# Optimization experiments

Measured on AMD Instinct MI355X. Metric: run time of the kernel, lower is better.

## Reference

```python
import math
import jax, jax.numpy as jnp
import numpy as np


def _scharr(img):
    # img: (..., H, W) -> (..., 2, H, W); F.conv2d is cross-correlation, as is lax.conv
    kx = jnp.array([[-3., 0., 3.], [10., 0., 10.], [-3., 0., 3.]], jnp.float32)
    k = jnp.stack([kx, kx.T])[:, None]  # (2,1,3,3)
    lead = img.shape[:-2]
    x = img.reshape((-1, 1) + img.shape[-2:])
    y = jax.lax.conv_general_dilated(x, k, (1, 1), 'SAME',
                                     dimension_numbers=('NCHW', 'OIHW', 'NCHW'))
    return y.reshape(lead + (2,) + img.shape[-2:])


def _rotate_nearest(x, angle_deg):
    # torchvision-style rotate with expand=True, nearest interpolation, zero fill
    H, W = x.shape[-2], x.shape[-1]
    a = math.radians(angle_deg)
    c, s = math.cos(a), math.sin(a)
    Hn = int(math.ceil(abs(W * s) + abs(H * c)))
    Wn = int(math.ceil(abs(W * c) + abs(H * s)))
    yy, xx = jnp.meshgrid(jnp.arange(Hn, dtype=jnp.float32),
                          jnp.arange(Wn, dtype=jnp.float32), indexing='ij')
    xg = xx - (Wn - 1) / 2.0
    yg = yy - (Hn - 1) / 2.0
    xi = c * xg - s * yg + (W - 1) / 2.0
    yi = s * xg + c * yg + (H - 1) / 2.0
    xn = jnp.round(xi).astype(jnp.int32)
    yn = jnp.round(yi).astype(jnp.int32)
    valid = (xn >= 0) & (xn < W) & (yn >= 0) & (yn < H)
    out = x[..., jnp.clip(yn, 0, H - 1), jnp.clip(xn, 0, W - 1)]
    return jnp.where(valid, out, jnp.zeros((), x.dtype))


def _gauss_derivs(img):
    # image_gaussian_derivatives: (B, C, H, W) -> (B, C, 8, H, W)
    H, W = img.shape[-2:]
    g = _scharr(img)  # (B, C, 2, H, W)
    # rotated_xywh(H, W, 45) to get crop offsets, exactly as in the source
    a = math.radians(45.0)
    al, be = math.cos(a), math.sin(a)
    cx, cy = W / 2.0, H / 2.0
    pts = [(0., 0.), (W - 1., 0.), (0., H - 1.), (W - 1., H - 1.)]
    rx = [al * px + be * py + (1 - al) * cx - be * cy for px, py in pts]
    ry = [-be * px + al * py + be * cx + (1 - al) * cy for px, py in pts]
    w45 = max(rx) - min(rx)
    h45 = max(ry) - min(ry)
    startx = int(max(0, (w45 - W) / 2))
    starty = int(max(0, (h45 - H) / 2))
    gr = _scharr(_rotate_nearest(img, 45.0))      # (B, C, 2, Hr, Wr)
    grb = _rotate_nearest(gr, -45.0)
    grc = grb[..., starty:starty + H, startx:startx + W]  # (B, C, 2, H, W)
    return jnp.concatenate([jnp.clip(g, 0, None), jnp.clip(g, None, 0),
                            jnp.clip(grc, 0, None), jnp.clip(grc, None, 0)], axis=-3)


def _normalize_min_max(x):
    hmin = x.min(axis=(-2, -1), keepdims=True)
    hmax = x.max(axis=(-2, -1), keepdims=True)
    return (x - hmin) / (hmax - hmin)


def _batched_hist(Z, nbins):
    # Z: (..., N) int in [0, nbins) -> per-row histogram (..., nbins) via one fused segment_sum
    lead = Z.shape[:-1]
    L = int(np.prod(lead))
    Zf = Z.reshape(L, -1)
    ids = (jnp.arange(L, dtype=jnp.int32)[:, None] * nbins + Zf).ravel()
    h = jax.ops.segment_sum(jnp.ones(ids.shape, jnp.float32), ids, num_segments=L * nbins)
    return h.reshape(lead + (nbins,))


def setup_inputs() -> dict:
    key = jax.random.key(0)
    k1, k2 = jax.random.split(key)
    img = jax.random.uniform(k1, (2, 3, 512, 512), jnp.float32)
    reg_lab = jax.random.randint(k2, (2, 1, 3, 512, 512), 0, 256, dtype=jnp.int32)
    return {'img': img, 'reg_lab': reg_lab,
            'color_bins': 25, 'texture_bins': 10, 'num_segments': 256}


def reference(img, reg_lab, color_bins, texture_bins, num_segments):
    B, I, G, H, W = reg_lab.shape
    C = img.shape[1]
    S = num_segments
    # normalized oriented gradient features (B, C, 8, H, W)
    tex = _normalize_min_max(_gauss_derivs(img))
    # region sizes: scatter_add of ones over region labels
    region_sizes = _batched_hist(reg_lab.reshape(B, I, G, H * W), S)  # (B,I,G,S)
    # color histograms
    Zc = (reg_lab[:, :, :, None].astype(jnp.float32) * color_bins
          + img[:, None, None] * (color_bins - 1)).astype(jnp.int32)  # (B,I,G,C,H,W)
    ch = _batched_hist(Zc.reshape(B, I, G, C, H * W), S * color_bins)
    ch = jnp.moveaxis(ch.reshape(B, I, G, C, S, color_bins), -2, -3)  # (B,I,G,S,C,cb)
    ch = ch / ch.sum(axis=(-2, -1), keepdims=True)
    # texture histograms
    Zt = (reg_lab[:, :, :, None, None].astype(jnp.float32) * texture_bins
          + tex[:, None, None] * (texture_bins - 1)).astype(jnp.int32)  # (B,I,G,C,8,H,W)
    th = _batched_hist(Zt.reshape(B, I, G, C, 8, H * W), S * texture_bins)
    th = jnp.moveaxis(th.reshape(B, I, G, C, 8, S, texture_bins), -2, -4)  # (B,I,G,S,C,8,tb)
    th = th / th.sum(axis=(-3, -2, -1), keepdims=True)
    # per-region bounding boxes via segment min/max (replaces the 5-deep python loop)
    grid_y, grid_x = jnp.meshgrid(jnp.arange(H, dtype=jnp.int32),
                                  jnp.arange(W, dtype=jnp.int32), indexing='ij')
    BIG = B * I * G
    ids = (jnp.arange(BIG, dtype=jnp.int32)[:, None] * S
           + reg_lab.reshape(BIG, H * W)).ravel()
    xs = jnp.tile(grid_x.ravel(), BIG)
    ys = jnp.tile(grid_y.ravel(), BIG)
    n = BIG * S
    xmin = jax.ops.segment_min(xs, ids, num_segments=n)
    xmax = jax.ops.segment_max(xs, ids, num_segments=n)
    ymin = jax.ops.segment_min(ys, ids, num_segments=n)
    ymax = jax.ops.segment_max(ys, ids, num_segments=n)
    nonempty = region_sizes.reshape(n) > 0
    xmin = jnp.where(nonempty, xmin, W)
    ymin = jnp.where(nonempty, ymin, H)
    xmax = jnp.where(nonempty, xmax, 0)
    ymax = jnp.where(nonempty, ymax, 0)
    xywh = jnp.stack([xmin, ymin, xmax - xmin, ymax - ymin], axis=-1).reshape(B, I, G, S, 4)
    return region_sizes, ch, th, xywh
```

## Files before the change

kernel.cpp:

```cpp
#include <hip/hip_runtime.h>
#include <climits>

#define HW 262144
#define IW 512
#define RN 725
#define NSEG 256
#define CH_OFF 1536
#define TH_OFF 116736
#define XY_OFF 485376
#define NBLK 256
#define THP 24
#define CHP 32

#define ASTR 67
#define RSTR 73
#define ROFF 156

static __device__ __forceinline__ float rtap_l(const float* __restrict__ Rt,
                                               int rx0, int ry0, int cx, int cy) {
    if (cx < 0 || cx >= RN || cy < 0 || cy >= RN) return 0.f;
    const float cs = 0.7071067811865476f;
    float xg = (float)cx - 362.0f;
    float yg = (float)cy - 362.0f;
    float xi = cs * xg - cs * yg + 255.5f;
    float yi = cs * xg + cs * yg + 255.5f;
    int xs = (int)rintf(xi);
    int ys = (int)rintf(yi);
    if (xs < 0 || xs >= IW || ys < 0 || ys >= IW) return 0.f;
    return Rt[(ys - ry0) * RSTR + (xs - rx0)];
}

static __device__ __forceinline__ void mm_of_map(const float* __restrict__ pmin,
                                                 const float* __restrict__ pmax,
                                                 int m, float* slo, float* shi,
                                                 float& mn, float& mx) {
    int tid = threadIdx.x;
    float lo = 3.4e38f, hi = -3.4e38f;
    for (int i = tid; i < NBLK; i += 256) {
        lo = fminf(lo, pmin[m * NBLK + i]);
        hi = fmaxf(hi, pmax[m * NBLK + i]);
    }
    slo[tid] = lo; shi[tid] = hi;
    __syncthreads();
    for (int off = 128; off > 0; off >>= 1) {
        if (tid < off) {
            slo[tid] = fminf(slo[tid], slo[tid + off]);
            shi[tid] = fmaxf(shi[tid], shi[tid + off]);
        }
        __syncthreads();
    }
    mn = slo[0]; mx = shi[0];
    __syncthreads();
}

__global__ __launch_bounds__(256) void k_front(
    const float* __restrict__ img, const int* __restrict__ lab,
    float* __restrict__ gmaps, float* __restrict__ pmin, float* __restrict__ pmax,
    unsigned char* __restrict__ lab8, unsigned* __restrict__ chp_w,
    unsigned* __restrict__ rsp, int* __restrict__ bxmin, int* __restrict__ bxmax,
    int* __restrict__ bymin, int* __restrict__ bymax)
{
    __shared__ __align__(16) unsigned char smem[20480];
    int bxid = blockIdx.x;
    int tid = threadIdx.x;
    int grp = bxid / 11, rem = bxid % 11;
    if (rem < 8) {
        int u = grp * 8 + rem;
        int tile = u & 255;
        int bc = u >> 8;
        float* At = (float*)smem;
        float* Rt = At + 18 * ASTR;
        float (*slo)[256] = (float (*)[256])(Rt + 24 * RSTR);
        float (*shi)[256] = slo + 4;
        {
            int i = tile * 256 + tid;
            int4 l = ((const int4*)(lab + (size_t)bc * HW))[i];
            unsigned v = (unsigned)(l.x & 255) | ((unsigned)(l.y & 255) << 8) |
                         ((unsigned)(l.z & 255) << 16) | ((unsigned)(l.w & 255) << 24);
            ((unsigned*)(lab8 + (size_t)bc * HW))[i] = v;
        }
        int tx0 = (tile & 7) << 6;
        int ty0 = (tile >> 3) << 4;
        const float* im = img + (size_t)bc * HW;
        int lane = tid & 63, wr = tid >> 6;
        for (int r = wr; r < 18; r += 4) {
            int gy = ty0 - 1 + r;
            bool yok = (gy >= 0 && gy < IW);
            int gx = tx0 - 1 + lane;
            At[r * ASTR + lane] = (yok && gx >= 0 && gx < IW) ? im[gy * IW + gx] : 0.f;
            if (lane < 2) {
                int gx2 = gx + 64;
                At[r * ASTR + lane + 64] = (yok && gx2 >= 0 && gx2 < IW) ? im[gy * IW + gx2] : 0.f;
            }
        }
        for (int r = wr; r < 24; r += 4) {
            int gy = ty0 - ROFF + r;
            bool yok = (gy >= 0 && gy < IW);
            int gx = tx0 - ROFF + lane;
            Rt[r * RSTR + lane] = (yok && gx >= 0 && gx < IW) ? im[gy * IW + gx] : 0.f;
            if (lane < 8) {
                int gx2 = gx + 64;
                Rt[r * RSTR + lane + 64] = (yok && gx2 >= 0 && gx2 < IW) ? im[gy * IW + gx2] : 0.f;
            }
        }
        __syncthreads();
        const float cs = 0.7071067811865476f;
        int rx0 = tx0 - ROFF, ry0 = ty0 - ROFF;
        float mn0 = 3.4e38f, mx0 = -3.4e38f, mn1 = 3.4e38f, mx1 = -3.4e38f;
        float mn2 = 3.4e38f, mx2 = -3.4e38f, mn3 = 3.4e38f, mx3 = -3.4e38f;
        #pragma unroll
        for (int it = 0; it < 4; ++it) {
            int ly = wr * 4 + it;
            int x = tx0 + lane, y = ty0 + ly;
            int p = y * IW + x;
            const float* Ar = At + ly * ASTR + lane;
            float a  = Ar[0],            b2 = Ar[1],            c2 = Ar[2];
            float d2 = Ar[ASTR],                                 e2 = Ar[ASTR + 2];
            float f2 = Ar[2 * ASTR],     h2 = Ar[2 * ASTR + 1], i9 = Ar[2 * ASTR + 2];
            float g0 = -3.f*a + 3.f*c2 + 10.f*d2 + 10.f*e2 - 3.f*f2 + 3.f*i9;
            float g1 = -3.f*a + 10.f*b2 - 3.f*c2 + 3.f*f2 + 10.f*h2 + 3.f*i9;
            gmaps[((size_t)(bc*2+0))*HW + p] = g0;
            gmaps[((size_t)(bc*2+1))*HW + p] = g1;
            float xgc = (float)(x + 105) - 512.5f;
            float ygc = (float)(y + 105) - 512.5f;
            float t1 = cs * xgc, t2 = cs * ygc;
            float xi = (t1 + t2) + 362.0f;
            float yi = (-t1 + t2) + 362.0f;
            int xn = (int)rintf(xi);
            int yn = (int)rintf(yi);
            float r0 = 0.f, r1 = 0.f;
            if (xn >= 0 && xn < RN && yn >= 0 && yn < RN) {
                float ra = rtap_l(Rt, rx0, ry0, xn-1, yn-1);
                float rb = rtap_l(Rt, rx0, ry0, xn,   yn-1);
                float rc = rtap_l(Rt, rx0, ry0, xn+1, yn-1);
                float rd = rtap_l(Rt, rx0, ry0, xn-1, yn);
                float re = rtap_l(Rt, rx0, ry0, xn+1, yn);
                float rf = rtap_l(Rt, rx0, ry0, xn-1, yn+1);
                float rh = rtap_l(Rt, rx0, ry0, xn,   yn+1);
                float ri = rtap_l(Rt, rx0, ry0, xn+1, yn+1);
                r0 = -3.f*ra + 3.f*rc + 10.f*rd + 10.f*re - 3.f*rf + 3.f*ri;
                r1 = -3.f*ra + 10.f*rb - 3.f*rc + 3.f*rf + 10.f*rh + 3.f*ri;
            }
            gmaps[((size_t)(12 + bc*2+0))*HW + p] = r0;
            gmaps[((size_t)(12 + bc*2+1))*HW + p] = r1;
            mn0 = fminf(mn0, g0); mx0 = fmaxf(mx0, g0);
            mn1 = fminf(mn1, g1); mx1 = fmaxf(mx1, g1);
            mn2 = fminf(mn2, r0); mx2 = fmaxf(mx2, r0);
            mn3 = fminf(mn3, r1); mx3 = fmaxf(mx3, r1);
        }
        slo[0][tid] = mn0; shi[0][tid] = mx0;
        slo[1][tid] = mn1; shi[1][tid] = mx1;
        slo[2][tid] = mn2; shi[2][tid] = mx2;
        slo[3][tid] = mn3; shi[3][tid] = mx3;
        __syncthreads();
        for (int off = 128; off > 0; off >>= 1) {
            if (tid < off) {
                #pragma unroll
                for (int k = 0; k < 4; ++k) {
                    slo[k][tid] = fminf(slo[k][tid], slo[k][tid + off]);
                    shi[k][tid] = fmaxf(shi[k][tid], shi[k][tid + off]);
                }
            }
            __syncthreads();
        }
        if (tid < 4) {
            int m = (tid < 2) ? (bc*2 + tid) : (12 + bc*2 + (tid - 2));
            pmin[m * NBLK + tile] = slo[tid][0];
            pmax[m * NBLK + tile] = shi[tid][0];
        }
    } else {
        int w = grp * 3 + (rem - 8);
        int gy = w >> 5;
        int sp = w & 31;
        int c = gy % 3;
        int bg = gy / 3;
        int b = bg / 3;
        unsigned* pk = (unsigned*)smem;
        unsigned* prc = pk + 3200;
        int* sxmin = (int*)(prc + 128);
        int* sxmax = sxmin + NSEG;
        int* symin = sxmax + NSEG;
        int* symax = symin + NSEG;
        bool do_reg = (c == 0);
        for (int i = tid; i < 3200; i += 256) pk[i] = 0;
        if (do_reg) {
            if (tid < 128) prc[tid] = 0;
            sxmin[tid] = INT_MAX; sxmax[tid] = INT_MIN;
            symin[tid] = INT_MAX; symax[tid] = INT_MIN;
        }
        __syncthreads();
        const float4* ip = (const float4*)(img + ((size_t)b * 3 + c) * HW);
        const int4* lp = (const int4*)(lab + (size_t)bg * HW);
        for (int i = sp * 256 + tid; i < HW / 4; i += 256 * CHP) {
            float4 v4 = ip[i];
            int4 l4 = lp[i];
            int l0 = l4.x & 255, l1 = l4.y & 255, l2 = l4.z & 255, l3 = l4.w & 255;
            int b0 = (int)((float)l0 * 25.0f + v4.x * 24.0f);
            int b1 = (int)((float)l1 * 25.0f + v4.y * 24.0f);
            int b2 = (int)((float)l2 * 25.0f + v4.z * 24.0f);
            int b3 = (int)((float)l3 * 25.0f + v4.w * 24.0f);
            b0 = min(max(b0, 0), 6399); b1 = min(max(b1, 0), 6399);
            b2 = min(max(b2, 0), 6399); b3 = min(max(b3, 0), 6399);
            atomicAdd(&pk[b0 >> 1], 1u << ((b0 & 1) << 4));
            atomicAdd(&pk[b1 >> 1], 1u << ((b1 & 1) << 4));
            atomicAdd(&pk[b2 >> 1], 1u << ((b2 & 1) << 4));
            atomicAdd(&pk[b3 >> 1], 1u << ((b3 & 1) << 4));
            if (do_reg) {
                int p = i << 2;
                int y = p >> 9, x = p & 511;
                atomicAdd(&prc[l0 >> 1], 1u << ((l0 & 1) << 4));
                atomicAdd(&prc[l1 >> 1], 1u << ((l1 & 1) << 4));
                atomicAdd(&prc[l2 >> 1], 1u << ((l2 & 1) << 4));
                atomicAdd(&prc[l3 >> 1], 1u << ((l3 & 1) << 4));
                atomicMin(&sxmin[l0], x);     atomicMax(&sxmax[l0], x);
                atomicMin(&sxmin[l1], x + 1); atomicMax(&sxmax[l1], x + 1);
                atomicMin(&sxmin[l2], x + 2); atomicMax(&sxmax[l2], x + 2);
                atomicMin(&sxmin[l3], x + 3); atomicMax(&sxmax[l3], x + 3);
                atomicMin(&symin[l0], y); atomicMax(&symax[l0], y);
                atomicMin(&symin[l1], y); atomicMax(&symax[l1], y);
                atomicMin(&symin[l2], y); atomicMax(&symax[l2], y);
                atomicMin(&symin[l3], y); atomicMax(&symax[l3], y);
            }
        }
        __syncthreads();
        unsigned* dst = chp_w + ((size_t)gy * CHP + sp) * 3200;
        for (int i = tid; i < 3200; i += 256) dst[i] = pk[i];
        if (do_reg) {
            size_t pi = (size_t)(bg * CHP + sp) * NSEG + tid;
            rsp[pi] = (prc[tid >> 1] >> ((tid & 1) << 4)) & 0xFFFFu;
            bxmin[pi] = sxmin[tid]; bxmax[pi] = sxmax[tid];
            bymin[pi] = symin[tid]; bymax[pi] = symax[tid];
        }
    }
}

__global__ __launch_bounds__(256) void k_thist(
    const float* __restrict__ maps, const unsigned char* __restrict__ lab8,
    const float* __restrict__ pmin, const float* __restrict__ pmax,
    unsigned* __restrict__ thp_w)
{
    __shared__ unsigned cnt[5120];
    __shared__ float slo[256], shi[256];
    int gy = blockIdx.y;
    int split = blockIdx.x;
    int gi = gy % 3;
    int r = gy / 3;
    int base = r & 1;
    int bd = r >> 1;
    int d = bd & 1;
    int bc = bd >> 1;
    int b = bc / 3;
    int m = base * 12 + bc * 2 + d;
    float mn, mx;
    mm_of_map(pmin, pmax, m, slo, shi, mn, mx);
    for (int i = threadIdx.x; i < 5120; i += 256) cnt[i] = 0;
    __syncthreads();
    float hminp = fmaxf(mn, 0.f), denp = fmaxf(mx, 0.f) - hminp;
    float hminn = fminf(mn, 0.f), denn = fminf(mx, 0.f) - hminn;
    const float4* src = (const float4*)(maps + (size_t)m * HW);
    const unsigned* lp = (const unsigned*)(lab8 + (size_t)(b * 3 + gi) * HW);
    for (int i = split * 256 + threadIdx.x; i < HW / 4; i += 256 * THP) {
        float4 v4 = src[i];
        unsigned l4 = lp[i];
#define TH1(V, SH)                                                     \
        {                                                              \
            float v = (V);                                             \
            bool ge = (v >= 0.f);                                      \
            float hm = ge ? hminp : hminn;                             \
            float dn = ge ? denp : denn;                               \
            float t9 = ((v - hm) / dn) * 9.0f;                         \
            int bi = (int)((float)((l4 >> SH) & 255u) * 10.0f + t9);   \
            bi = min(max(bi, 0), 2559);                                \
            atomicAdd(&cnt[(ge ? 0 : 2560) + bi], 1u);                 \
        }
        TH1(v4.x, 0) TH1(v4.y, 8) TH1(v4.z, 16) TH1(v4.w, 24)
#undef TH1
    }
    __syncthreads();
    unsigned* dst = thp_w + ((size_t)(gy * THP + split)) * 2560;
    for (int i = threadIdx.x; i < 2560; i += 256)
        dst[i] = cnt[2 * i] | (cnt[2 * i + 1] << 16);
}

__global__ __launch_bounds__(256) void k_final(
    const unsigned* __restrict__ thp_w, const unsigned* __restrict__ chp_w,
    const unsigned* __restrict__ rsp,
    const int* __restrict__ bxmin, const int* __restrict__ bxmax,
    const int* __restrict__ bymin, const int* __restrict__ bymax,
    const float* __restrict__ pmin, const float* __restrict__ pmax,
    float* __restrict__ out)
{
    int tid = threadIdx.x;
    int bx = blockIdx.x;
    if (bx < 288) {
        __shared__ unsigned hist[1280];
        __shared__ unsigned srs[64];
        __shared__ float slo[256], shi[256];
        int gy = bx >> 2;
        int ck = bx & 3;
        int l0 = ck << 6;
        int gi = gy % 3; int r = gy / 3; int base = r & 1;
        int bd = r >> 1; int d = bd & 1; int bc = bd >> 1;
        int b = bc / 3, c = bc - b * 3;
        int m = base * 12 + bc * 2 + d;
        int bg = b * 3 + gi;
        float mn, mx;
        mm_of_map(pmin, pmax, m, slo, shi, mn, mx);
        for (int w = tid; w < 640; w += 256) {
            int gw = (w < 320) ? (l0 * 5 + w) : (1280 + l0 * 5 + (w - 320));
            unsigned s0 = 0, s1 = 0;
            #pragma unroll 4
            for (int p = 0; p < THP; ++p) {
                unsigned v = thp_w[((size_t)(gy * THP + p)) * 2560 + gw];
                s0 += v & 0xFFFFu; s1 += v >> 16;
            }
            int bi = (w < 320) ? (2 * w) : (640 + 2 * (w - 320));
            hist[bi] = s0; hist[bi + 1] = s1;
        }
        if (tid < 64) {
            unsigned s = 0;
            #pragma unroll 4
            for (int p = 0; p < CHP; ++p) s += rsp[((size_t)(bg * CHP + p)) * NSEG + l0 + tid];
            srs[tid] = s;
        }
        __syncthreads();
        if (tid < 64) {
            int l = l0 + tid;
            unsigned nge = 0;
            for (int tb = 0; tb < 10; ++tb) nge += hist[tid * 10 + tb];
            unsigned rsu = srs[tid];
            unsigned nlt = (rsu >= nge) ? (rsu - nge) : 0u;
            float hminp = fmaxf(mn, 0.f), denp = fmaxf(mx, 0.f) - hminp;
            float hminn = fminf(mn, 0.f), denn = fminf(mx, 0.f) - hminn;
            float la = (float)l;
            float tp0 = ((0.0f - hminp) / denp) * 9.0f;
            float tn0 = ((0.0f - hminn) / denn) * 9.0f;
            int g0off = l0 * 10;
            int bp = (int)(la * 10.0f + tp0); bp = min(max(bp, 0), 2559);
            int bn = (int)(la * 10.0f + tn0); bn = min(max(bn, 0), 2559);
            if (nlt && bp >= g0off && bp < g0off + 640) atomicAdd(&hist[bp - g0off], nlt);
            if (nge && bn >= g0off && bn < g0off + 640) atomicAdd(&hist[640 + bn - g0off], nge);
        }
        __syncthreads();
        for (int i = tid; i < 1280; i += 256) {
            int pos = (i < 640);
            int rr = pos ? i : i - 640;
            int lseg = rr / 10, tb = rr % 10;
            int seg = l0 + lseg;
            int tt = base * 4 + (pos ? 0 : 2) + d;
            float rsf = (float)srs[lseg];
            out[TH_OFF + ((size_t)(bg * NSEG + seg) * 3 + c) * 80 + tt * 10 + tb] =
                (float)hist[i] / (24.0f * rsf);
        }
    } else {
        __shared__ unsigned crs[CHP];
        __shared__ int sxm[CHP], sxM[CHP], sym[CHP], syM[CHP];
        int seg = bx - 288;
        int bg = seg >> 8;
        int s = seg & 255;
        if (tid < CHP) crs[tid] = rsp[((size_t)(bg * CHP + tid)) * NSEG + s];
        else if (tid < 2 * CHP) sxm[tid - CHP] = bxmin[((size_t)(bg * CHP + tid - CHP)) * NSEG + s];
        else if (tid < 3 * CHP) sxM[tid - 2 * CHP] = bxmax[((size_t)(bg * CHP + tid - 2 * CHP)) * NSEG + s];
        else if (tid < 4 * CHP) sym[tid - 3 * CHP] = bymin[((size_t)(bg * CHP + tid - 3 * CHP)) * NSEG + s];
        else if (tid < 5 * CHP) syM[tid - 4 * CHP] = bymax[((size_t)(bg * CHP + tid - 4 * CHP)) * NSEG + s];
        __syncthreads();
        if (tid < 75) {
            unsigned rs = 0;
            #pragma unroll 4
            for (int p = 0; p < CHP; ++p) rs += crs[p];
            float rsf = (float)rs;
            int c = tid / 25, cb = tid - c * 25;
            int bin = s * 25 + cb;
            unsigned sum = 0;
            #pragma unroll 4
            for (int p = 0; p < CHP; ++p) {
                unsigned v = chp_w[((size_t)((bg * 3 + c) * CHP + p)) * 3200 + (bin >> 1)];
                sum += (v >> ((bin & 1) << 4)) & 0xFFFFu;
            }
            out[CH_OFF + (size_t)seg * 75 + tid] = (float)sum / (3.0f * rsf);
        } else if (tid == 75) {
            unsigned rs = 0;
            #pragma unroll 4
            for (int p = 0; p < CHP; ++p) rs += crs[p];
            float rsf = (float)rs;
            out[seg] = rsf;
            int xmn = INT_MAX, xmx = INT_MIN, ymn = INT_MAX, ymx = INT_MIN;
            #pragma unroll 4
            for (int p = 0; p < CHP; ++p) {
                xmn = min(xmn, sxm[p]); xmx = max(xmx, sxM[p]);
                ymn = min(ymn, sym[p]); ymx = max(ymx, syM[p]);
            }
            if (!(rsf > 0.f)) { xmn = IW; ymn = IW; xmx = 0; ymx = 0; }
            float* xy = out + XY_OFF + (size_t)seg * 4;
            xy[0] = (float)xmn; xy[1] = (float)ymn;
            xy[2] = (float)(xmx - xmn); xy[3] = (float)(ymx - ymn);
        }
    }
}

extern "C" void kernel_launch(void* const* d_in, const int* in_sizes, int n_in,
                              void* d_out, int out_size, void* d_ws, size_t ws_size,
                              hipStream_t stream) {
    const float* img = (const float*)d_in[0];
    const int* lab = (const int*)d_in[1];
    float* out = (float*)d_out;

    float* gmaps = (float*)d_ws;
    float* pmin = gmaps + (size_t)24 * HW;
    float* pmax = pmin + 24 * NBLK;
    unsigned* thp_w = (unsigned*)(pmax + 24 * NBLK);
    unsigned* chp_w = thp_w + (size_t)72 * THP * 2560;
    unsigned char* lab8 = (unsigned char*)(chp_w + (size_t)18 * CHP * 3200);
    unsigned* rsp = (unsigned*)(lab8 + (size_t)6 * HW);
    int* bxmin = (int*)(rsp + 6 * CHP * NSEG);
    int* bxmax = bxmin + 6 * CHP * NSEG;
    int* bymin = bxmax + 6 * CHP * NSEG;
    int* bymax = bymin + 6 * CHP * NSEG;

    hipLaunchKernelGGL(k_front, dim3(2112), dim3(256), 0, stream,
                       img, lab, gmaps, pmin, pmax, lab8, chp_w, rsp, bxmin, bxmax, bymin, bymax);
    hipLaunchKernelGGL(k_thist, dim3(THP, 72), dim3(256), 0, stream, gmaps, lab8, pmin, pmax, thp_w);
    hipLaunchKernelGGL(k_final, dim3(288 + 1536), dim3(256), 0, stream,
                       thp_w, chp_w, rsp, bxmin, bxmax, bymin, bymax, pmin, pmax, out);
}
```

Measured before the change: 119.9 us.

## Move color-hist finalization into texture-hist kernel, split final into smaller blocks

The color-histogram, region-size and bounding-box finalization, which only depends on the front kernel, now runs as extra blocks inside the texture-histogram kernel, so it overlaps with texture binning instead of waiting behind it. Each of those blocks now handles two segments instead of one, halving the block count. The remaining texture finalize kernel uses 32-segment chunks, giving 576 blocks instead of 288 for more parallelism. Shared memory is a single union buffer sized for the larger branch, which may lower occupancy for the light finalize blocks.

```diff
diff --git a/kernel.cpp b/kernel.cpp
--- a/kernel.cpp
+++ b/kernel.cpp
@@ -234,142 +234,93 @@
     }
 }
 
-__global__ __launch_bounds__(256) void k_thist(
+__global__ __launch_bounds__(256) void k_hist(
     const float* __restrict__ maps, const unsigned char* __restrict__ lab8,
     const float* __restrict__ pmin, const float* __restrict__ pmax,
-    unsigned* __restrict__ thp_w)
-{
-    __shared__ unsigned cnt[5120];
-    __shared__ float slo[256], shi[256];
-    int gy = blockIdx.y;
-    int split = blockIdx.x;
-    int gi = gy % 3;
-    int r = gy / 3;
-    int base = r & 1;
-    int bd = r >> 1;
-    int d = bd & 1;
-    int bc = bd >> 1;
-    int b = bc / 3;
-    int m = base * 12 + bc * 2 + d;
-    float mn, mx;
-    mm_of_map(pmin, pmax, m, slo, shi, mn, mx);
-    for (int i = threadIdx.x; i < 5120; i += 256) cnt[i] = 0;
-    __syncthreads();
-    float hminp = fmaxf(mn, 0.f), denp = fmaxf(mx, 0.f) - hminp;
-    float hminn = fminf(mn, 0.f), denn = fminf(mx, 0.f) - hminn;
-    const float4* src = (const float4*)(maps + (size_t)m * HW);
-    const unsigned* lp = (const unsigned*)(lab8 + (size_t)(b * 3 + gi) * HW);
-    for (int i = split * 256 + threadIdx.x; i < HW / 4; i += 256 * THP) {
-        float4 v4 = src[i];
-        unsigned l4 = lp[i];
-#define TH1(V, SH)                                                     \
-        {                                                              \
-            float v = (V);                                             \
-            bool ge = (v >= 0.f);                                      \
-            float hm = ge ? hminp : hminn;                             \
-            float dn = ge ? denp : denn;                               \
-            float t9 = ((v - hm) / dn) * 9.0f;                         \
-            int bi = (int)((float)((l4 >> SH) & 255u) * 10.0f + t9);   \
-            bi = min(max(bi, 0), 2559);                                \
-            atomicAdd(&cnt[(ge ? 0 : 2560) + bi], 1u);                 \
-        }
-        TH1(v4.x, 0) TH1(v4.y, 8) TH1(v4.z, 16) TH1(v4.w, 24)
-#undef TH1
-    }
-    __syncthreads();
-    unsigned* dst = thp_w + ((size_t)(gy * THP + split)) * 2560;
-    for (int i = threadIdx.x; i < 2560; i += 256)
-        dst[i] = cnt[2 * i] | (cnt[2 * i + 1] << 16);
-}
-
-__global__ __launch_bounds__(256) void k_final(
-    const unsigned* __restrict__ thp_w, const unsigned* __restrict__ chp_w,
+    unsigned* __restrict__ thp_w, const unsigned* __restrict__ chp_w,
     const unsigned* __restrict__ rsp,
     const int* __restrict__ bxmin, const int* __restrict__ bxmax,
     const int* __restrict__ bymin, const int* __restrict__ bymax,
-    const float* __restrict__ pmin, const float* __restrict__ pmax,
     float* __restrict__ out)
 {
+    __shared__ __align__(16) unsigned char smem[22528];
+    int bx = blockIdx.x;
     int tid = threadIdx.x;
-    int bx = blockIdx.x;
-    if (bx < 288) {
-        __shared__ unsigned hist[1280];
-        __shared__ unsigned srs[64];
-        __shared__ float slo[256], shi[256];
-        int gy = bx >> 2;
-        int ck = bx & 3;
-        int l0 = ck << 6;
-        int gi = gy % 3; int r = gy / 3; int base = r & 1;
-        int bd = r >> 1; int d = bd & 1; int bc = bd >> 1;
-        int b = bc / 3, c = bc - b * 3;
+    if (bx < 1728) {
+        unsigned* cnt = (unsigned*)smem;
+        float* slo = (float*)(smem + 20480);
+        float* shi = slo + 256;
+        int gy = bx / THP;
+        int split = bx - gy * THP;
+        int gi = gy % 3;
+        int r = gy / 3;
+        int base = r & 1;
+        int bd = r >> 1;
+        int d = bd & 1;
+        int bc = bd >> 1;
+        int b = bc / 3;
         int m = base * 12 + bc * 2 + d;
-        int bg = b * 3 + gi;
         float mn, mx;
         mm_of_map(pmin, pmax, m, slo, shi, mn, mx);
-        for (int w = tid; w < 640; w += 256) {
-            int gw = (w < 320) ? (l0 * 5 + w) : (1280 + l0 * 5 + (w - 320));
-            unsigned s0 = 0, s1 = 0;
-            #pragma unroll 4
-            for (int p = 0; p < THP; ++p) {
-                unsigned v = thp_w[((size_t)(gy * THP + p)) * 2560 + gw];
-                s0 += v & 0xFFFFu; s1 += v >> 16;
-            }
-            int bi = (w < 320) ? (2 * w) : (640 + 2 * (w - 320));
-            hist[bi] = s0; hist[bi + 1] = s1;
-        }
-        if (tid < 64) {
-            unsigned s = 0;
-            #pragma unroll 4
-            for (int p = 0; p < CHP; ++p) s += rsp[((size_t)(bg * CHP + p)) * NSEG + l0 + tid];
-            srs[tid] = s;
-        }
-        __syncthreads();
-        if (tid < 64) {
-            int l = l0 + tid;
-            unsigned nge = 0;
-            for (int tb = 0; tb < 10; ++tb) nge += hist[tid * 10 + tb];
-            unsigned rsu = srs[tid];
-            unsigned nlt = (rsu >= nge) ? (rsu - nge) : 0u;
-            float hminp = fmaxf(mn, 0.f), denp = fmaxf(mx, 0.f) - hminp;
-            float hminn = fminf(mn, 0.f), denn = fminf(mx, 0.f) - hminn;
-            float la = (float)l;
-            float tp0 = ((0.0f - hminp) / denp) * 9.0f;
-            float tn0 = ((0.0f - hminn) / denn) * 9.0f;
-            int g0off = l0 * 10;
-            int bp = (int)(la * 10.0f + tp0); bp = min(max(bp, 0), 2559);
-            int bn = (int)(la * 10.0f + tn0); bn = min(max(bn, 0), 2559);
-            if (nlt && bp >= g0off && bp < g0off + 640) atomicAdd(&hist[bp - g0off], nlt);
-            if (nge && bn >= g0off && bn < g0off + 640) atomicAdd(&hist[640 + bn - g0off], nge);
-        }
-        __syncthreads();
-        for (int i = tid; i < 1280; i += 256) {
-            int pos = (i < 640);
-            int rr = pos ? i : i - 640;
-            int lseg = rr / 10, tb = rr % 10;
-            int seg = l0 + lseg;
-            int tt = base * 4 + (pos ? 0 : 2) + d;
-            float rsf = (float)srs[lseg];
-            out[TH_OFF + ((size_t)(bg * NSEG + seg) * 3 + c) * 80 + tt * 10 + tb] =
-                (float)hist[i] / (24.0f * rsf);
-        }
+        for (int i = tid; i < 5120; i += 256) cnt[i] = 0;
+        __syncthreads();
+        float hminp = fmaxf(mn, 0.f), denp = fmaxf(mx, 0.f) - hminp;
+        float hminn = fminf(mn, 0.f), denn = fminf(mx, 0.f) - hminn;
+        const float4* src = (const float4*)(maps + (size_t)m * HW);
+        const unsigned* lp = (const unsigned*)(lab8 + (size_t)(b * 3 + gi) * HW);
+        for (int i = split * 256 + tid; i < HW / 4; i += 256 * THP) {
+            float4 v4 = src[i];
+            unsigned l4 = lp[i];
+#define TH1(V, SH)                                                     \
+            {                                                          \
+                float v = (V);                                         \
+                bool ge = (v >= 0.f);                                  \
+                float hm = ge ? hminp : hminn;                         \
+                float dn = ge ? denp : denn;                           \
+                float t9 = ((v - hm) / dn) * 9.0f;                     \
+                int bi = (int)((float)((l4 >> SH) & 255u) * 10.0f + t9); \
+                bi = min(max(bi, 0), 2559);                            \
+                atomicAdd(&cnt[(ge ? 0 : 2560) + bi], 1u);             \
+            }
+            TH1(v4.x, 0) TH1(v4.y, 8) TH1(v4.z, 16) TH1(v4.w, 24)
+#undef TH1
+        }
+        __syncthreads();
+        unsigned* dst = thp_w + ((size_t)(gy * THP + split)) * 2560;
+        for (int i = tid; i < 2560; i += 256)
+            dst[i] = cnt[2 * i] | (cnt[2 * i + 1] << 16);
     } else {
-        __shared__ unsigned crs[CHP];
-        __shared__ int sxm[CHP], sxM[CHP], sym[CHP], syM[CHP];
-        int seg = bx - 288;
-        int bg = seg >> 8;
-        int s = seg & 255;
-        if (tid < CHP) crs[tid] = rsp[((size_t)(bg * CHP + tid)) * NSEG + s];
-        else if (tid < 2 * CHP) sxm[tid - CHP] = bxmin[((size_t)(bg * CHP + tid - CHP)) * NSEG + s];
-        else if (tid < 3 * CHP) sxM[tid - 2 * CHP] = bxmax[((size_t)(bg * CHP + tid - 2 * CHP)) * NSEG + s];
-        else if (tid < 4 * CHP) sym[tid - 3 * CHP] = bymin[((size_t)(bg * CHP + tid - 3 * CHP)) * NSEG + s];
-        else if (tid < 5 * CHP) syM[tid - 4 * CHP] = bymax[((size_t)(bg * CHP + tid - 4 * CHP)) * NSEG + s];
-        __syncthreads();
-        if (tid < 75) {
+        unsigned (*crs)[32] = (unsigned (*)[32])smem;
+        int (*sxm)[32] = (int (*)[32])(smem + 256);
+        int (*sxM)[32] = (int (*)[32])(smem + 512);
+        int (*sym)[32] = (int (*)[32])(smem + 768);
+        int (*syM)[32] = (int (*)[32])(smem + 1024);
+        int j = bx - 1728;
+        int seg0 = j * 2;
+        int bg = seg0 >> 8;
+        int s0 = seg0 & 255, s1 = s0 + 1;
+        int g = tid >> 5, w = tid & 31;
+        size_t base0 = (size_t)(bg * CHP + w) * NSEG;
+        if (g == 0)      crs[0][w] = rsp[base0 + s0];
+        else if (g == 1) sxm[0][w] = bxmin[base0 + s0];
+        else if (g == 2) sxM[0][w] = bxmax[base0 + s0];
+        else if (g == 3) sym[0][w] = bymin[base0 + s0];
+        else if (g == 4) syM[0][w] = bymax[base0 + s0];
+        else if (g == 5) crs[1][w] = rsp[base0 + s1];
+        else if (g == 6) sxm[1][w] = bxmin[base0 + s1];
+        else if (g == 7) sxM[1][w] = bxmax[base0 + s1];
+        if (g == 0)      sym[1][w] = bymin[base0 + s1];
+        else if (g == 1) syM[1][w] = bymax[base0 + s1];
+        __syncthreads();
+        int half = tid >> 7, t2 = tid & 127;
+        int s = half ? s1 : s0;
+        int seg = seg0 + half;
+        if (t2 < 75) {
             unsigned rs = 0;
             #pragma unroll 4
-            for (int p = 0; p < CHP; ++p) rs += crs[p];
+            for (int p = 0; p < CHP; ++p) rs += crs[half][p];
             float rsf = (float)rs;
-            int c = tid / 25, cb = tid - c * 25;
+            int c = t2 / 25, cb = t2 - c * 25;
             int bin = s * 25 + cb;
             unsigned sum = 0;
             #pragma unroll 4
@@ -377,24 +328,92 @@
                 unsigned v = chp_w[((size_t)((bg * 3 + c) * CHP + p)) * 3200 + (bin >> 1)];
                 sum += (v >> ((bin & 1) << 4)) & 0xFFFFu;
             }
-            out[CH_OFF + (size_t)seg * 75 + tid] = (float)sum / (3.0f * rsf);
-        } else if (tid == 75) {
+            out[CH_OFF + (size_t)seg * 75 + t2] = (float)sum / (3.0f * rsf);
+        } else if (t2 == 75) {
             unsigned rs = 0;
             #pragma unroll 4
-            for (int p = 0; p < CHP; ++p) rs += crs[p];
+            for (int p = 0; p < CHP; ++p) rs += crs[half][p];
             float rsf = (float)rs;
             out[seg] = rsf;
             int xmn = INT_MAX, xmx = INT_MIN, ymn = INT_MAX, ymx = INT_MIN;
             #pragma unroll 4
             for (int p = 0; p < CHP; ++p) {
-                xmn = min(xmn, sxm[p]); xmx = max(xmx, sxM[p]);
-                ymn = min(ymn, sym[p]); ymx = max(ymx, syM[p]);
+                xmn = min(xmn, sxm[half][p]); xmx = max(xmx, sxM[half][p]);
+                ymn = min(ymn, sym[half][p]); ymx = max(ymx, syM[half][p]);
             }
             if (!(rsf > 0.f)) { xmn = IW; ymn = IW; xmx = 0; ymx = 0; }
             float* xy = out + XY_OFF + (size_t)seg * 4;
             xy[0] = (float)xmn; xy[1] = (float)ymn;
             xy[2] = (float)(xmx - xmn); xy[3] = (float)(ymx - ymn);
         }
+    }
+}
+
+__global__ __launch_bounds__(256) void k_final(
+    const unsigned* __restrict__ thp_w, const unsigned* __restrict__ rsp,
+    const float* __restrict__ pmin, const float* __restrict__ pmax,
+    float* __restrict__ out)
+{
+    __shared__ unsigned hist[640];
+    __shared__ unsigned srs[32];
+    __shared__ float slo[256], shi[256];
+    int tid = threadIdx.x;
+    int bx = blockIdx.x;
+    int gy = bx >> 3;
+    int ck = bx & 7;
+    int l0 = ck << 5;
+    int gi = gy % 3; int r = gy / 3; int base = r & 1;
+    int bd = r >> 1; int d = bd & 1; int bc = bd >> 1;
+    int b = bc / 3, c = bc - b * 3;
+    int m = base * 12 + bc * 2 + d;
+    int bg = b * 3 + gi;
+    float mn, mx;
+    mm_of_map(pmin, pmax, m, slo, shi, mn, mx);
+    for (int w = tid; w < 320; w += 256) {
+        int gw = (w < 160) ? (l0 * 5 + w) : (1280 + l0 * 5 + (w - 160));
+        unsigned s0 = 0, s1 = 0;
+        #pragma unroll 4
+        for (int p = 0; p < THP; ++p) {
+            unsigned v = thp_w[((size_t)(gy * THP + p)) * 2560 + gw];
+            s0 += v & 0xFFFFu; s1 += v >> 16;
+        }
+        int bi = (w < 160) ? (2 * w) : (320 + 2 * (w - 160));
+        hist[bi] = s0; hist[bi + 1] = s1;
+    }
+    if (tid < 32) {
+        unsigned s = 0;
+        #pragma unroll 4
+        for (int p = 0; p < CHP; ++p) s += rsp[((size_t)(bg * CHP + p)) * NSEG + l0 + tid];
+        srs[tid] = s;
+    }
+    __syncthreads();
+    if (tid < 32) {
+        int l = l0 + tid;
+        unsigned nge = 0;
+        for (int tb = 0; tb < 10; ++tb) nge += hist[tid * 10 + tb];
+        unsigned rsu = srs[tid];
+        unsigned nlt = (rsu >= nge) ? (rsu - nge) : 0u;
+        float hminp = fmaxf(mn, 0.f), denp = fmaxf(mx, 0.f) - hminp;
+        float hminn = fminf(mn, 0.f), denn = fminf(mx, 0.f) - hminn;
+        float la = (float)l;
+        float tp0 = ((0.0f - hminp) / denp) * 9.0f;
+        float tn0 = ((0.0f - hminn) / denn) * 9.0f;
+        int g0off = l0 * 10;
+        int bp = (int)(la * 10.0f + tp0); bp = min(max(bp, 0), 2559);
+        int bn = (int)(la * 10.0f + tn0); bn = min(max(bn, 0), 2559);
+        if (nlt && bp >= g0off && bp < g0off + 320) atomicAdd(&hist[bp - g0off], nlt);
+        if (nge && bn >= g0off && bn < g0off + 320) atomicAdd(&hist[320 + bn - g0off], nge);
+    }
+    __syncthreads();
+    for (int i = tid; i < 640; i += 256) {
+        int pos = (i < 320);
+        int rr = pos ? i : i - 320;
+        int lseg = rr / 10, tb = rr % 10;
+        int seg = l0 + lseg;
+        int tt = base * 4 + (pos ? 0 : 2) + d;
+        float rsf = (float)srs[lseg];
+        out[TH_OFF + ((size_t)(bg * NSEG + seg) * 3 + c) * 80 + tt * 10 + tb] =
+            (float)hist[i] / (24.0f * rsf);
     }
 }
 
@@ -419,7 +438,8 @@
 
     hipLaunchKernelGGL(k_front, dim3(2112), dim3(256), 0, stream,
                        img, lab, gmaps, pmin, pmax, lab8, chp_w, rsp, bxmin, bxmax, bymin, bymax);
-    hipLaunchKernelGGL(k_thist, dim3(THP, 72), dim3(256), 0, stream, gmaps, lab8, pmin, pmax, thp_w);
-    hipLaunchKernelGGL(k_final, dim3(288 + 1536), dim3(256), 0, stream,
-                       thp_w, chp_w, rsp, bxmin, bxmax, bymin, bymax, pmin, pmax, out);
-}
+    hipLaunchKernelGGL(k_hist, dim3(1728 + 768), dim3(256), 0, stream,
+                       gmaps, lab8, pmin, pmax, thp_w, chp_w, rsp, bxmin, bxmax, bymin, bymax, out);
+    hipLaunchKernelGGL(k_final, dim3(576), dim3(256), 0, stream,
+                       thp_w, rsp, pmin, pmax, out);
+}
```

Measured after the change: 116.2 us, median of 2. -3.1%, faster.
